# Optimization experiments

Hardware: AMD Instinct MI355X
Metric: run time of the kernel (lower is better)

The kernel has to match this reference:

```python
import jax, jax.numpy as jnp
import numpy as np

B, N, J = 2, 2048, 2048
DIM, HEADS, DH = 1024, 16, 64
INNER = HEADS * DH          # 1024
FF_INNER = 4 * DIM          # 4096
EPS = 1e-5


def layernorm(x, g, b):
    mu = jnp.mean(x, axis=-1, keepdims=True)
    var = jnp.var(x, axis=-1, keepdims=True)
    return (x - mu) * jax.lax.rsqrt(var + EPS) * g + b


def setup_inputs() -> dict:
    key = jax.random.key(0)
    ks = jax.random.split(key, 8)
    s = 0.02
    return {
        "x": jax.random.normal(ks[0], (B, N, DIM), jnp.float32),
        "context": jax.random.normal(ks[1], (B, J, DIM), jnp.float32),
        "norm_g": jnp.ones((DIM,), jnp.float32),
        "norm_b": jnp.zeros((DIM,), jnp.float32),
        "cnorm_g": jnp.ones((DIM,), jnp.float32),
        "cnorm_b": jnp.zeros((DIM,), jnp.float32),
        "Wq": jax.random.normal(ks[2], (DIM, INNER), jnp.float32) * s,
        "Wkv": jax.random.normal(ks[3], (DIM, 2 * DH), jnp.float32) * s,
        "Wo": jax.random.normal(ks[4], (INNER, DIM), jnp.float32) * s,
        "Wff1": jax.random.normal(ks[5], (DIM, 2 * FF_INNER), jnp.float32) * s,
        "Wff2": jax.random.normal(ks[6], (FF_INNER, DIM), jnp.float32) * s,
    }


def reference(x, context, norm_g, norm_b, cnorm_g, cnorm_b, Wq, Wkv, Wo, Wff1, Wff2):
    scale = DH ** -0.5
    xn = layernorm(x, norm_g, norm_b)                      # [b, n, dim]
    cn = layernorm(context, cnorm_g, cnorm_b)              # [b, j, dim]

    q = (xn @ Wq).reshape(B, N, HEADS, DH) * scale         # [b, n, h, dh]
    kv = cn @ Wkv                                          # [b, j, 2*dh]
    k, v = kv[..., :DH], kv[..., DH:]                      # shared across heads (MQA)

    sim = jnp.einsum('bihd,bjd->bhij', q, k)               # [b, h, n, j]
    attn = jax.nn.softmax(sim, axis=-1)                    # amax-stabilized internally
    out = jnp.einsum('bhij,bjd->bihd', attn, v)            # [b, n, h, dh]
    out = out.reshape(B, N, INNER) @ Wo                    # [b, n, dim]

    # parallel SwiGLU FF on the normed input, residual-added
    ff = xn @ Wff1                                         # [b, n, 2*ff_inner]
    a, gate = ff[..., :FF_INNER], ff[..., FF_INNER:]
    out = out + (jax.nn.silu(gate) * a) @ Wff2
    return out
```

## Files before the change

kernel.cpp:

```cpp
#include <hip/hip_runtime.h>
#include <stdint.h>

typedef unsigned short u16;
typedef __attribute__((ext_vector_type(8))) short short8;
typedef __attribute__((ext_vector_type(4))) float f32x4;
typedef __attribute__((ext_vector_type(16))) float f32x16;

#define GPTR(p) ((const __attribute__((address_space(1))) void*)(p))
#define SPTR(p) ((__attribute__((address_space(3))) void*)(p))
#define GLDS16(g, l) __builtin_amdgcn_global_load_lds(GPTR(g), SPTR(l), 16, 0, 0)

static __device__ __forceinline__ float bf2f(u16 u) {
  union { unsigned int i; float f; } c; c.i = ((unsigned int)u) << 16; return c.f;
}
static __device__ __forceinline__ u16 f2bf(float f) {
  union { float f; unsigned int u; } c; c.f = f;
  unsigned int r = 0x7fffu + ((c.u >> 16) & 1u);
  return (u16)((c.u + r) >> 16);
}
static __device__ __forceinline__ unsigned cvtpk(float a, float b) {
  unsigned r;
  asm volatile("v_cvt_pk_bf16_f32 %0, %1, %2" : "=v"(r) : "v"(a), "v"(b));
  return r;
}
static __device__ __forceinline__ int swz4(int row, int c) { return c ^ ((row >> 1) & 3); }

__global__ __launch_bounds__(256) void ln_kernel(
    const float* __restrict__ x, const float* __restrict__ ctx,
    const float* __restrict__ g, const float* __restrict__ b,
    const float* __restrict__ cg, const float* __restrict__ cb,
    u16* __restrict__ xn, u16* __restrict__ cn)
{
  const int row = blockIdx.x;
  const float* src; const float* gg; const float* bb; u16* dst;
  if (row < 4096) { src = x + (size_t)row * 1024; gg = g;  bb = b;  dst = xn + (size_t)row * 1024; }
  else            { src = ctx + (size_t)(row - 4096) * 1024; gg = cg; bb = cb; dst = cn + (size_t)(row - 4096) * 1024; }
  const int t = threadIdx.x;
  float4 v = *(const float4*)&src[t * 4];
  float s  = v.x + v.y + v.z + v.w;
  float s2 = v.x * v.x + v.y * v.y + v.z * v.z + v.w * v.w;
  #pragma unroll
  for (int off = 1; off < 64; off <<= 1) { s += __shfl_xor(s, off); s2 += __shfl_xor(s2, off); }
  __shared__ float ls[4], ls2[4];
  const int w = t >> 6;
  if ((t & 63) == 0) { ls[w] = s; ls2[w] = s2; }
  __syncthreads();
  s  = ls[0] + ls[1] + ls[2] + ls[3];
  s2 = ls2[0] + ls2[1] + ls2[2] + ls2[3];
  const float mu   = s * (1.0f / 1024.0f);
  const float var  = s2 * (1.0f / 1024.0f) - mu * mu;
  const float rstd = rsqrtf(var + 1e-5f);
  float xv[4] = { v.x, v.y, v.z, v.w };
  u16 o[4];
  #pragma unroll
  for (int i = 0; i < 4; ++i)
    o[i] = f2bf((xv[i] - mu) * rstd * gg[t * 4 + i] + bb[t * 4 + i]);
  uint2 pv;
  pv.x = (unsigned)o[0] | ((unsigned)o[1] << 16);
  pv.y = (unsigned)o[2] | ((unsigned)o[3] << 16);
  *(uint2*)&dst[t * 4] = pv;
}

__global__ __launch_bounds__(256) void transpose_k(
    const float* __restrict__ in, u16* __restrict__ out, int R, int C, int ldo, float scale)
{
  __shared__ float tile[64][65];
  const int c0 = blockIdx.x * 64, r0 = blockIdx.y * 64;
  const int t = threadIdx.x;
  const int tr = t >> 4, tc = (t & 15) * 4;
  #pragma unroll
  for (int i = 0; i < 4; ++i) {
    int r = tr + i * 16;
    float4 v = *(const float4*)&in[(size_t)(r0 + r) * C + c0 + tc];
    tile[r][tc + 0] = v.x; tile[r][tc + 1] = v.y; tile[r][tc + 2] = v.z; tile[r][tc + 3] = v.w;
  }
  __syncthreads();
  #pragma unroll
  for (int i = 0; i < 2; ++i) {
    int c  = (t >> 3) + i * 32;
    int rb = (t & 7) * 8;
    union { u16 s[8]; uint4 v; } pk;
    #pragma unroll
    for (int u = 0; u < 8; ++u) pk.s[u] = f2bf(tile[rb + u][c] * scale);
    *(uint4*)&out[(size_t)(c0 + c) * ldo + r0 + rb] = pk.v;
  }
}

__global__ __launch_bounds__(256) void transpose_ff1(
    const float* __restrict__ in, u16* __restrict__ out)
{
  __shared__ float tile[64][65];
  const int c0 = blockIdx.x * 64, r0 = blockIdx.y * 64;
  const int t = threadIdx.x;
  const int tr = t >> 4, tc = (t & 15) * 4;
  #pragma unroll
  for (int i = 0; i < 4; ++i) {
    int r = tr + i * 16;
    float4 v = *(const float4*)&in[(size_t)(r0 + r) * 8192 + c0 + tc];
    tile[r][tc + 0] = v.x; tile[r][tc + 1] = v.y; tile[r][tc + 2] = v.z; tile[r][tc + 3] = v.w;
  }
  __syncthreads();
  #pragma unroll
  for (int i = 0; i < 2; ++i) {
    int c  = (t >> 3) + i * 32;
    int rb = (t & 7) * 8;
    const int gc = c0 + c;
    int j, add16;
    if (gc < 4096) { j = gc; add16 = 0; } else { j = gc - 4096; add16 = 16; }
    const int row = ((j >> 7) << 8) + (((j >> 5) & 3) << 6) + (((j >> 4) & 1) << 5) + add16 + (j & 15);
    union { u16 s[8]; uint4 v; } pk;
    #pragma unroll
    for (int u = 0; u < 8; ++u) pk.s[u] = f2bf(tile[rb + u][c]);
    *(uint4*)&out[(size_t)row * 1024 + r0 + rb] = pk.v;
  }
}

#define MM32(MQ, M, NN) acc[MQ][M][NN] = __builtin_amdgcn_mfma_f32_16x16x32_bf16(af##M, bf##NN, acc[MQ][M][NN], 0, 0, 0)
#define MFMA16_32(MQ) \
  MM32(MQ,0,0); MM32(MQ,0,1); MM32(MQ,0,2); MM32(MQ,0,3); \
  MM32(MQ,1,0); MM32(MQ,1,1); MM32(MQ,1,2); MM32(MQ,1,3); \
  MM32(MQ,2,0); MM32(MQ,2,1); MM32(MQ,2,2); MM32(MQ,2,3); \
  MM32(MQ,3,0); MM32(MQ,3,1); MM32(MQ,3,2); MM32(MQ,3,3)

#define SA32(SBUF, H, KT) GLDS16(gA32[H] + ((size_t)(KT) << 5), SBUF + (size_t)((H) * 64 + w16o) * 32)
#define SB32(SBUF, H, KT) GLDS16(gB32[H] + ((size_t)(KT) << 5), SBUF + (size_t)((H) * 128 + w16o2) * 32)

#define DSB32(PB_) do { \
  bf0 = *(const short8*)(PB_ + 0    + cks); bf1 = *(const short8*)(PB_ + 512  + cks); \
  bf2 = *(const short8*)(PB_ + 1024 + cks); bf3 = *(const short8*)(PB_ + 1536 + cks); \
} while (0)

#define PC32(PA_, MQ, STAGE_STMT, GATE_STMT) do { \
  af0 = *(const short8*)(PA_ + (MQ) * 2048 + 0    + cks); \
  af1 = *(const short8*)(PA_ + (MQ) * 2048 + 512  + cks); \
  af2 = *(const short8*)(PA_ + (MQ) * 2048 + 1024 + cks); \
  af3 = *(const short8*)(PA_ + (MQ) * 2048 + 1536 + cks); \
  STAGE_STMT; \
  __builtin_amdgcn_s_barrier(); \
  asm volatile("s_waitcnt lgkmcnt(0)" ::: "memory"); \
  __builtin_amdgcn_s_setprio(1); \
  MFMA16_32(MQ); \
  __builtin_amdgcn_s_setprio(0); \
  GATE_STMT; \
  __builtin_amdgcn_s_barrier(); \
} while (0)

#define GATE3 asm volatile("s_waitcnt vmcnt(3)" ::: "memory")
#define GATE0 asm volatile("s_waitcnt vmcnt(0)" ::: "memory")

__global__ __launch_bounds__(512, 2) void gemm32_ff(
    const u16* __restrict__ A, const u16* __restrict__ BT, u16* __restrict__ Ho,
    int M, int N, int Ktot)
{
  __shared__ u16 sh[2][2][8192];
  const int nbm = M >> 8;
  const int nwg = gridDim.x;
  const int bid = blockIdx.x;
  const int o = (bid & 7) * (nwg >> 3) + (bid >> 3);
  const int bm = o % nbm, bn = o / nbm;
  const int NI = Ktot >> 6;

  const int t = threadIdx.x, w = t >> 6, lane = t & 63;
  const int wr = w >> 2, wc = w & 3;
  const int lr = lane & 15, lg = lane >> 4;
  const int l4 = lane >> 2, sl = lane & 3;
  const int w16o  = w * 16 + ((w >= 4) ? 64 : 0);
  const int w16o2 = w * 16;

  const u16* gA32[2]; const u16* gB32[2];
  #pragma unroll
  for (int h = 0; h < 2; ++h) {
    const int rowA = h * 64 + w16o + l4;
    gA32[h] = A + (size_t)(bm * 256 + rowA) * Ktot + (size_t)((sl ^ ((rowA >> 1) & 3)) * 8);
    const int rowB = h * 128 + w16o2 + l4;
    gB32[h] = BT + (size_t)(bn * 256 + rowB) * Ktot + (size_t)((sl ^ ((rowB >> 1) & 3)) * 8);
  }
  u16* sA0 = &sh[0][0][0]; u16* sA1 = &sh[1][0][0];
  u16* sB0 = &sh[0][1][0]; u16* sB1 = &sh[1][1][0];
  const int cks = (lg ^ ((lr >> 1) & 3)) * 8;
  const u16* pA_b0 = sA0 + (wr * 128 + lr) * 32;
  const u16* pA_b1 = sA1 + (wr * 128 + lr) * 32;
  const u16* pB_b0 = sB0 + (wc * 64 + lr) * 32;
  const u16* pB_b1 = sB1 + (wc * 64 + lr) * 32;

  f32x4 acc[2][4][4];
  const f32x4 z4 = { 0.f, 0.f, 0.f, 0.f };
  #pragma unroll
  for (int a = 0; a < 2; ++a)
    #pragma unroll
    for (int b = 0; b < 4; ++b)
      #pragma unroll
      for (int c = 0; c < 4; ++c) acc[a][b][c] = z4;
  short8 af0, af1, af2, af3;
  short8 bf0, bf1, bf2, bf3;

  SA32(sA0, 0, 0); SA32(sA0, 1, 0); SB32(sB0, 0, 0); SB32(sB0, 1, 0);
  SB32(sB1, 0, 1); SB32(sB1, 1, 1); SA32(sA1, 0, 1);
  GATE3;
  __builtin_amdgcn_s_barrier();

  for (int i = 0; i < NI; ++i) {
    const bool st = (i < NI - 1);
    const int X = 2 * i + 2, Y = 2 * i + 3;
    DSB32(pB_b0);
    PC32(pA_b0, 0, SA32(sA1, 1, 2 * i + 1), );
    PC32(pA_b0, 1,
         if (st) { SB32(sB0, 0, X); SB32(sB0, 1, X); SA32(sA0, 0, X); },
         if (st) { GATE3; } else { GATE0; });
    DSB32(pB_b1);
    PC32(pA_b1, 0, if (st) { SA32(sA0, 1, X); }, );
    PC32(pA_b1, 1,
         if (st) { SB32(sB1, 0, Y); SB32(sB1, 1, Y); SA32(sA1, 0, Y); },
         if (st) { GATE3; });
  }

  const int colb = 1024 + bn * 128 + wc * 32 + lr;
  #pragma unroll
  for (int mq = 0; mq < 2; ++mq)
    #pragma unroll
    for (int m = 0; m < 4; ++m)
      #pragma unroll
      for (int rr = 0; rr < 4; ++rr) {
        const int row = bm * 256 + wr * 128 + mq * 64 + m * 16 + lg * 4 + rr;
        #pragma unroll
        for (int n2 = 0; n2 < 2; ++n2) {
          const float a = acc[mq][m][2 * n2][rr];
          const float gt = acc[mq][m][2 * n2 + 1][rr];
          const float h = a * gt / (1.0f + __expf(-gt));
          Ho[(size_t)row * 5120 + colb + n2 * 16] = f2bf(h);
        }
      }
}

#define MM1(MQ, M, NN, BF) acc[MQ][M][NN] = __builtin_amdgcn_mfma_f32_16x16x32_bf16(af##M, BF, acc[MQ][M][NN], 0, 0, 0)
#define MFMA16(MQ, KS) \
  MM1(MQ,0,0,bf##KS##0); MM1(MQ,0,1,bf##KS##1); MM1(MQ,0,2,bf##KS##2); MM1(MQ,0,3,bf##KS##3); \
  MM1(MQ,1,0,bf##KS##0); MM1(MQ,1,1,bf##KS##1); MM1(MQ,1,2,bf##KS##2); MM1(MQ,1,3,bf##KS##3); \
  MM1(MQ,2,0,bf##KS##0); MM1(MQ,2,1,bf##KS##1); MM1(MQ,2,2,bf##KS##2); MM1(MQ,2,3,bf##KS##3); \
  MM1(MQ,3,0,bf##KS##0); MM1(MQ,3,1,bf##KS##1); MM1(MQ,3,2,bf##KS##2); MM1(MQ,3,3,bf##KS##3)

#define SG_A(SBUF, H, KT) do { \
    GLDS16(gA[H][0] + ((size_t)(KT) << 6), SBUF + ((H) * 64 + w16o) * 64); \
    GLDS16(gA[H][1] + ((size_t)(KT) << 6), SBUF + ((H) * 64 + w16o + 8) * 64); \
  } while (0)
#define SG_B(SBUF, H, KT) do { \
    GLDS16(gB[H][0] + ((size_t)(KT) << 6), SBUF + ((H) * 128 + w16o2) * 64); \
    GLDS16(gB[H][1] + ((size_t)(KT) << 6), SBUF + ((H) * 128 + w16o2 + 8) * 64); \
  } while (0)

#define DS_B(PB_) do { \
  bf00 = *(const short8*)(PB_ + 0    + cks0); bf01 = *(const short8*)(PB_ + 1024 + cks0); \
  bf02 = *(const short8*)(PB_ + 2048 + cks0); bf03 = *(const short8*)(PB_ + 3072 + cks0); \
  bf10 = *(const short8*)(PB_ + 0    + cks1); bf11 = *(const short8*)(PB_ + 1024 + cks1); \
  bf12 = *(const short8*)(PB_ + 2048 + cks1); bf13 = *(const short8*)(PB_ + 3072 + cks1); \
} while (0)

#define P_CORE(PA_, MQ, KS, STAGE_STMT, PREB_STMT, GATE_STMT) do { \
  af0 = *(const short8*)(PA_ + (MQ) * 4096 + 0    + cks##KS); \
  af1 = *(const short8*)(PA_ + (MQ) * 4096 + 1024 + cks##KS); \
  af2 = *(const short8*)(PA_ + (MQ) * 4096 + 2048 + cks##KS); \
  af3 = *(const short8*)(PA_ + (MQ) * 4096 + 3072 + cks##KS); \
  STAGE_STMT; \
  PREB_STMT; \
  __builtin_amdgcn_s_barrier(); \
  asm volatile("s_waitcnt lgkmcnt(0)" ::: "memory"); \
  __builtin_amdgcn_s_setprio(1); \
  MFMA16(MQ, KS); \
  __builtin_amdgcn_s_setprio(0); \
  GATE_STMT; \
  __builtin_amdgcn_s_barrier(); \
} while (0)

#define GATE6 asm volatile("s_waitcnt vmcnt(6)" ::: "memory")
#define HINT8 asm volatile("s_waitcnt lgkmcnt(8)" ::: "memory")

__global__ __launch_bounds__(512, 2) void gemm64_sk(
    const u16* __restrict__ A, const u16* __restrict__ BT, u16* __restrict__ C,
    int M, int N, int Ktot, int Kslice)
{
  __shared__ u16 sh[2][2][16384];
  const int nbn = N >> 8;
  const int nwg = gridDim.x;
  const int bid = blockIdx.x;
  const int o = (bid & 7) * (nwg >> 3) + (bid >> 3);
  const int bn = o % nbn, bm = o / nbn;
  const int kbase = blockIdx.y * Kslice;
  const int NI = Kslice >> 7;

  const int t = threadIdx.x, w = t >> 6, lane = t & 63;
  const int wr = w >> 2, wc = w & 3;
  const int lr = lane & 15, lg = lane >> 4;
  const int r8 = lane >> 3, ch = lane & 7;
  const int clog = ch ^ r8;
  const int w16o  = w * 16 + ((w >= 4) ? 64 : 0);
  const int w16o2 = w * 16;

  const u16* gA[2][2]; const u16* gB[2][2];
  #pragma unroll
  for (int h = 0; h < 2; ++h)
    #pragma unroll
    for (int qq = 0; qq < 2; ++qq) {
      gA[h][qq] = A  + (size_t)(bm * 256 + h * 64  + w16o  + qq * 8 + r8) * Ktot + kbase + clog * 8;
      gB[h][qq] = BT + (size_t)(bn * 256 + h * 128 + w16o2 + qq * 8 + r8) * Ktot + kbase + clog * 8;
    }
  u16* sA0 = &sh[0][0][0]; u16* sA1 = &sh[1][0][0];
  u16* sB0 = &sh[0][1][0]; u16* sB1 = &sh[1][1][0];
  const int cks0 = ((0 + lg) ^ (lr & 7)) * 8;
  const int cks1 = ((4 + lg) ^ (lr & 7)) * 8;
  const u16* pA_b0 = sA0 + (wr * 128 + lr) * 64;
  const u16* pA_b1 = sA1 + (wr * 128 + lr) * 64;
  const u16* pB_b0 = sB0 + (wc * 64 + lr) * 64;
  const u16* pB_b1 = sB1 + (wc * 64 + lr) * 64;

  f32x4 acc[2][4][4];
  const f32x4 z4 = { 0.f, 0.f, 0.f, 0.f };
  #pragma unroll
  for (int a = 0; a < 2; ++a)
    #pragma unroll
    for (int b = 0; b < 4; ++b)
      #pragma unroll
      for (int c = 0; c < 4; ++c) acc[a][b][c] = z4;
  short8 af0, af1, af2, af3;
  short8 bf00, bf01, bf02, bf03, bf10, bf11, bf12, bf13;

  SG_B(sB0, 0, 0); SG_B(sB0, 1, 0); SG_A(sA0, 0, 0); SG_A(sA0, 1, 0);
  SG_B(sB1, 0, 1); SG_B(sB1, 1, 1); SG_A(sA1, 0, 1);
  GATE6;
  __builtin_amdgcn_s_barrier();

  for (int i = 0; i < NI; ++i) {
    const int k2 = 2 * i;
    const bool st = (i < NI - 1);
    DS_B(pB_b0);
    P_CORE(pA_b0, 0, 0, SG_A(sA1, 1, k2 + 1), HINT8, );
    P_CORE(pA_b0, 1, 0, if (st) SG_B(sB0, 0, k2 + 2), , );
    P_CORE(pA_b0, 0, 1, if (st) SG_B(sB0, 1, k2 + 2), , );
    P_CORE(pA_b0, 1, 1, if (st) SG_A(sA0, 0, k2 + 2), ,
           if (st) { GATE6; } else { GATE0; });
    DS_B(pB_b1);
    P_CORE(pA_b1, 0, 0, if (st) SG_A(sA0, 1, k2 + 2), HINT8, );
    P_CORE(pA_b1, 1, 0, if (st) SG_B(sB1, 0, k2 + 3), , );
    P_CORE(pA_b1, 0, 1, if (st) SG_B(sB1, 1, k2 + 3), , );
    P_CORE(pA_b1, 1, 1, if (st) SG_A(sA1, 0, k2 + 3), ,
           if (st) { GATE6; });
  }

  u16* Co = C + (size_t)blockIdx.y * M * N;
  #pragma unroll
  for (int mq = 0; mq < 2; ++mq)
    #pragma unroll
    for (int m = 0; m < 4; ++m)
      #pragma unroll
      for (int n = 0; n < 4; ++n)
        #pragma unroll
        for (int rr = 0; rr < 4; ++rr) {
          const int row = bm * 256 + wr * 128 + mq * 64 + m * 16 + lg * 4 + rr;
          const int col = bn * 256 + wc * 64 + n * 16 + lr;
          Co[(size_t)row * N + col] = f2bf(acc[mq][m][n][rr]);
        }
}

__global__ __launch_bounds__(256) void gemm_bt_sk(
    const u16* __restrict__ A, const u16* __restrict__ BT, u16* __restrict__ Cp,
    int M, int N, int Kslice, int Ktot)
{
  __shared__ u16 As[128 * 32];
  __shared__ u16 Bs[128 * 32];
  const int bm = blockIdx.y, bn = blockIdx.x, z = blockIdx.z;
  const int t = threadIdx.x;
  const int w = t >> 6, lane = t & 63;
  const int wr = w >> 1, wc = w & 1;
  const int lr = lane & 15, lkc = lane >> 4;

  f32x4 acc[4][4];
  const f32x4 z4 = { 0.f, 0.f, 0.f, 0.f };
  #pragma unroll
  for (int mi = 0; mi < 4; ++mi)
    #pragma unroll
    for (int ni = 0; ni < 4; ++ni) acc[mi][ni] = z4;

  const int kbase = z * Kslice;
  const int i0 = t, i1 = t + 256;
  const int r0 = i0 >> 2, k0 = swz4(r0, i0 & 3) * 8;
  const int r1 = i1 >> 2, k1 = swz4(r1, i1 & 3) * 8;
  const u16* a0 = A + (size_t)(bm * 128 + r0) * Ktot + kbase + k0;
  const u16* a1 = A + (size_t)(bm * 128 + r1) * Ktot + kbase + k1;
  const u16* b0 = BT + (size_t)(bn * 128 + r0) * Ktot + kbase + k0;
  const u16* b1 = BT + (size_t)(bn * 128 + r1) * Ktot + kbase + k1;
  u16* As0 = As + (size_t)w * 512;
  u16* As1 = As + (size_t)(w + 4) * 512;
  u16* Bs0 = Bs + (size_t)w * 512;
  u16* Bs1 = Bs + (size_t)(w + 4) * 512;

  const int nk = Kslice >> 5;
  for (int kt = 0; kt < nk; ++kt) {
    __syncthreads();
    GLDS16(a0, As0); GLDS16(a1, As1); GLDS16(b0, Bs0); GLDS16(b1, Bs1);
    a0 += 32; a1 += 32; b0 += 32; b1 += 32;
    __syncthreads();
    short8 af[4], bf[4];
    #pragma unroll
    for (int mi = 0; mi < 4; ++mi) {
      int row = wr * 64 + mi * 16 + lr;
      af[mi] = *(const short8*)&As[row * 32 + swz4(row, lkc) * 8];
    }
    #pragma unroll
    for (int ni = 0; ni < 4; ++ni) {
      int row = wc * 64 + ni * 16 + lr;
      bf[ni] = *(const short8*)&Bs[row * 32 + swz4(row, lkc) * 8];
    }
    #pragma unroll
    for (int mi = 0; mi < 4; ++mi)
      #pragma unroll
      for (int ni = 0; ni < 4; ++ni)
        acc[mi][ni] = __builtin_amdgcn_mfma_f32_16x16x32_bf16(af[mi], bf[ni], acc[mi][ni], 0, 0, 0);
  }

  u16* Cz = Cp + (size_t)z * M * N;
  const int row0 = bm * 128 + wr * 64, col0 = bn * 128 + wc * 64;
  const int rsub = (lane >> 4) * 4;
  #pragma unroll
  for (int mi = 0; mi < 4; ++mi)
    #pragma unroll
    for (int ni = 0; ni < 4; ++ni)
      #pragma unroll
      for (int r = 0; r < 4; ++r)
        Cz[(size_t)(row0 + mi * 16 + rsub + r) * N + (col0 + ni * 16 + lr)] = f2bf(acc[mi][ni][r]);
}

__global__ __launch_bounds__(256) void reduce_kv(const u16* __restrict__ part, u16* __restrict__ out)
{
  const size_t base = ((size_t)blockIdx.x * 256 + threadIdx.x) * 8;
  float s[8] = { 0.f, 0.f, 0.f, 0.f, 0.f, 0.f, 0.f, 0.f };
  #pragma unroll
  for (int zz = 0; zz < 8; ++zz) {
    const short8 v = *(const short8*)&part[(size_t)zz * 524288 + base];
    #pragma unroll
    for (int i = 0; i < 8; ++i) s[i] += bf2f((u16)v[i]);
  }
  union { u16 o[8]; uint4 v; } pk;
  #pragma unroll
  for (int i = 0; i < 8; ++i) pk.o[i] = f2bf(s[i]);
  *(uint4*)&out[base] = pk.v;
}

__global__ __launch_bounds__(256) void reduce_out(const u16* __restrict__ part, float* __restrict__ out)
{
  const size_t base = ((size_t)blockIdx.x * 256 + threadIdx.x) * 8;
  float s[8] = { 0.f, 0.f, 0.f, 0.f, 0.f, 0.f, 0.f, 0.f };
  #pragma unroll
  for (int zz = 0; zz < 4; ++zz) {
    const short8 v = *(const short8*)&part[(size_t)zz * 4194304 + base];
    #pragma unroll
    for (int i = 0; i < 8; ++i) s[i] += bf2f((u16)v[i]);
  }
  f32x4 lo = { s[0], s[1], s[2], s[3] };
  f32x4 hi = { s[4], s[5], s[6], s[7] };
  *(f32x4*)&out[base] = lo;
  *(f32x4*)&out[base + 4] = hi;
}

__global__ __launch_bounds__(256) void attn_kernel(
    const u16* __restrict__ q, const u16* __restrict__ kv, u16* __restrict__ o)
{
  __shared__ u16 Ks[128 * 64];
  __shared__ u16 Vt[64 * 128];
  __shared__ u16 Ps[4][32 * 128];
  const int b = blockIdx.z, hb = blockIdx.y, qb = blockIdx.x;
  const int t = threadIdx.x, w = t >> 6, lane = t & 63;
  const int q32 = lane & 31, hl = lane >> 5;
  const int hd = hb * 4 + w;

  const size_t qbase = (size_t)b * 2048 + qb * 64;
  short8 qa[2][4];
  #pragma unroll
  for (int t32 = 0; t32 < 2; ++t32)
    #pragma unroll
    for (int dq = 0; dq < 4; ++dq)
      qa[t32][dq] = *(const short8*)&q[(qbase + t32 * 32 + q32) * 1024 + hd * 64 + dq * 16 + hl * 8];

  f32x16 oacc[2][2];
  #pragma unroll
  for (int i = 0; i < 2; ++i)
    #pragma unroll
    for (int j = 0; j < 2; ++j)
      #pragma unroll
      for (int r = 0; r < 16; ++r) oacc[i][j][r] = 0.f;
  float m_[2] = { -1e30f, -1e30f }, l_[2] = { 0.f, 0.f };

  const size_t kvb = (size_t)b * 2048 * 128;
  const int vd0 = (t & 7) * 8;
  const int vodd = (t >> 3) & 1;
  u16* Pw = &Ps[w][0];

  uint4 vhold[4];
  #pragma unroll
  for (int c = 0; c < 4; ++c) {
    const int vj = (c * 256 + t) >> 3;
    vhold[c] = *(const uint4*)&kv[kvb + (size_t)vj * 128 + 64 + vd0];
  }

  for (int jt = 0; jt < 16; ++jt) {
    __syncthreads();
    #pragma unroll
    for (int n = 0; n < 4; ++n) {
      const int cc = n * 256 + w * 64;
      const int ccl = cc + lane;
      const int row = ccl >> 3, lc = (ccl & 7) ^ (row & 7);
      GLDS16(&kv[kvb + (size_t)(jt * 128 + row) * 128 + lc * 8], Ks + (size_t)cc * 8);
    }
    #pragma unroll
    for (int c = 0; c < 4; ++c) {
      const int seg = c * 256 + t;
      const int vj = seg >> 3;
      const int jp = vj >> 1;
      const uint4 vv = vhold[c];
      uint4 pvv;
      pvv.x = __shfl_xor((int)vv.x, 8);
      pvv.y = __shfl_xor((int)vv.y, 8);
      pvv.z = __shfl_xor((int)vv.z, 8);
      pvv.w = __shfl_xor((int)vv.w, 8);
      const unsigned ow[4] = { vv.x, vv.y, vv.z, vv.w };
      const unsigned pw[4] = { pvv.x, pvv.y, pvv.z, pvv.w };
      if (!vodd) {
        #pragma unroll
        for (int u = 0; u < 4; ++u) {
          const int d = vd0 + u;
          const unsigned own = (u & 1) ? (ow[u >> 1] >> 16) : (ow[u >> 1] & 0xffffu);
          const unsigned par = (u & 1) ? (pw[u >> 1] >> 16) : (pw[u >> 1] & 0xffffu);
          const int byteoff = d * 256 + ((4 * jp) ^ (((d & 7) ^ ((d >> 3) & 7)) << 4));
          *(unsigned*)((char*)Vt + byteoff) = own | (par << 16);
        }
      } else {
        #pragma unroll
        for (int u = 0; u < 4; ++u) {
          const int ue = u + 4;
          const int d = vd0 + ue;
          const unsigned own = (ue & 1) ? (ow[ue >> 1] >> 16) : (ow[ue >> 1] & 0xffffu);
          const unsigned par = (ue & 1) ? (pw[ue >> 1] >> 16) : (pw[ue >> 1] & 0xffffu);
          const int byteoff = d * 256 + ((4 * jp) ^ (((d & 7) ^ ((d >> 3) & 7)) << 4));
          *(unsigned*)((char*)Vt + byteoff) = par | (own << 16);
        }
      }
    }
    __builtin_amdgcn_sched_barrier(0);
    if (jt < 15) {
      #pragma unroll
      for (int c = 0; c < 4; ++c) {
        const int vj = (c * 256 + t) >> 3;
        vhold[c] = *(const uint4*)&kv[kvb + (size_t)((jt + 1) * 128 + vj) * 128 + 64 + vd0];
      }
      asm volatile("s_waitcnt vmcnt(4) lgkmcnt(0)" ::: "memory");
    } else {
      asm volatile("s_waitcnt vmcnt(0) lgkmcnt(0)" ::: "memory");
    }
    __builtin_amdgcn_s_barrier();
    __builtin_amdgcn_sched_barrier(0);

    #pragma unroll
    for (int t32 = 0; t32 < 2; ++t32) {
      f32x16 s[4];
      #pragma unroll
      for (int j32 = 0; j32 < 4; ++j32)
        #pragma unroll
        for (int r = 0; r < 16; ++r) s[j32][r] = 0.f;
      __builtin_amdgcn_s_setprio(1);
      #pragma unroll
      for (int j32 = 0; j32 < 4; ++j32) {
        const int row = j32 * 32 + q32;
        #pragma unroll
        for (int dq = 0; dq < 4; ++dq) {
          const int slot = (dq * 2 + hl) ^ (row & 7);
          const short8 kf = *(const short8*)&Ks[row * 64 + slot * 8];
          s[j32] = __builtin_amdgcn_mfma_f32_32x32x16_bf16(kf, qa[t32][dq], s[j32], 0, 0, 0);
        }
      }
      __builtin_amdgcn_s_setprio(0);
      float mt = -1e30f;
      #pragma unroll
      for (int j32 = 0; j32 < 4; ++j32)
        #pragma unroll
        for (int r = 0; r < 16; ++r) mt = fmaxf(mt, s[j32][r]);
      mt = fmaxf(mt, __shfl_xor(mt, 32));
      const bool noresc = (bool)__all(mt <= m_[t32] + 8.0f);
      float nm = m_[t32];
      if (!noresc) {
        nm = fmaxf(m_[t32], mt);
        const float alpha = __expf(m_[t32] - nm);
        m_[t32] = nm;
        l_[t32] *= alpha;
        #pragma unroll
        for (int d32 = 0; d32 < 2; ++d32)
          #pragma unroll
          for (int r = 0; r < 16; ++r) oacc[t32][d32][r] *= alpha;
      }
      float lsum = 0.f;
      #pragma unroll
      for (int j32 = 0; j32 < 4; ++j32) {
        float p[16];
        #pragma unroll
        for (int r = 0; r < 16; ++r) { p[r] = __expf(s[j32][r] - nm); lsum += p[r]; }
        #pragma unroll
        for (int g = 0; g < 4; ++g) {
          const unsigned lo = cvtpk(p[4 * g + 0], p[4 * g + 1]);
          const unsigned hi = cvtpk(p[4 * g + 2], p[4 * g + 3]);
          const int j2 = j32 * 64 + 16 * g + 8 * hl;
          const int byteoff = q32 * 256 + (j2 ^ ((q32 & 7) << 4));
          uint2 wv; wv.x = lo; wv.y = hi;
          *(uint2*)((char*)Pw + byteoff) = wv;
        }
      }
      lsum += __shfl_xor(lsum, 32);
      l_[t32] += lsum;
      short8 pf[8];
      #pragma unroll
      for (int kk = 0; kk < 8; ++kk) {
        const int byteoff = q32 * 256 + ((kk * 32 + hl * 16) ^ ((q32 & 7) << 4));
        pf[kk] = *(const short8*)((const char*)Pw + byteoff);
      }
      __builtin_amdgcn_s_setprio(1);
      #pragma unroll
      for (int d32 = 0; d32 < 2; ++d32) {
        const int dr = d32 * 32 + q32;
        const int vswz = ((dr & 7) ^ ((dr >> 3) & 7)) << 4;
        #pragma unroll
        for (int kk = 0; kk < 8; ++kk) {
          const int byteoff = dr * 256 + ((kk * 32 + hl * 16) ^ vswz);
          const short8 vf = *(const short8*)((const char*)Vt + byteoff);
          oacc[t32][d32] = __builtin_amdgcn_mfma_f32_32x32x16_bf16(vf, pf[kk], oacc[t32][d32], 0, 0, 0);
        }
      }
      __builtin_amdgcn_s_setprio(0);
    }
  }

  float* Ot = (float*)Pw;
  #pragma unroll
  for (int t32 = 0; t32 < 2; ++t32) {
    const float inv = 1.0f / l_[t32];
    #pragma unroll
    for (int d32 = 0; d32 < 2; ++d32) {
      #pragma unroll
      for (int r = 0; r < 16; ++r) {
        const int d = (r & 3) + 8 * (r >> 2) + 4 * hl;
        const int byteoff = q32 * 128 + ((4 * d) ^ ((q32 & 7) << 4));
        *(float*)((char*)Ot + byteoff) = oacc[t32][d32][r] * inv;
      }
      const int qr = lane >> 1, dc = (lane & 1) * 16;
      union { u16 s[16]; uint4 v[2]; } ob;
      #pragma unroll
      for (int cch = 0; cch < 4; ++cch) {
        const int byteoff = qr * 128 + ((4 * (dc + 4 * cch)) ^ ((qr & 7) << 4));
        const f32x4 vv = *(const f32x4*)((const char*)Ot + byteoff);
        ob.s[cch * 4 + 0] = f2bf(vv[0]);
        ob.s[cch * 4 + 1] = f2bf(vv[1]);
        ob.s[cch * 4 + 2] = f2bf(vv[2]);
        ob.s[cch * 4 + 3] = f2bf(vv[3]);
      }
      u16* orow = &o[(qbase + t32 * 32 + qr) * 5120 + hd * 64 + d32 * 32 + dc];
      *(uint4*)orow = ob.v[0];
      *(uint4*)(orow + 8) = ob.v[1];
    }
  }
}

extern "C" void kernel_launch(void* const* d_in, const int* in_sizes, int n_in,
                              void* d_out, int out_size, void* d_ws, size_t ws_size,
                              hipStream_t stream)
{
  const float* x    = (const float*)d_in[0];
  const float* ctx  = (const float*)d_in[1];
  const float* ng   = (const float*)d_in[2];
  const float* nb   = (const float*)d_in[3];
  const float* cg   = (const float*)d_in[4];
  const float* cb   = (const float*)d_in[5];
  const float* Wq   = (const float*)d_in[6];
  const float* Wkv  = (const float*)d_in[7];
  const float* Wo   = (const float*)d_in[8];
  const float* Wff1 = (const float*)d_in[9];
  const float* Wff2 = (const float*)d_in[10];

  u16* p = (u16*)d_ws;
  u16* WqT   = p; p += (size_t)1024 * 1024;
  u16* W2T   = p; p += (size_t)8192 * 1024;
  u16* WkvT  = p; p += (size_t)128 * 1024;
  u16* WcT   = p; p += (size_t)1024 * 5120;
  u16* kvbuf = p; p += (size_t)4096 * 128;
  u16* aoh   = p; p += (size_t)4096 * 5120;
  u16* xn    = p; p += (size_t)4096 * 1024;
  u16* cn    = p; p += (size_t)4096 * 1024;
  u16* qbuf  = p; p += (size_t)4096 * 1024;
  u16* kvpart = W2T;
  u16* ffpart = xn;
  (void)in_sizes; (void)n_in; (void)out_size; (void)ws_size;

  ln_kernel<<<8192, 256, 0, stream>>>(x, ctx, ng, nb, cg, cb, xn, cn);

  transpose_k<<<dim3(16, 16),  256, 0, stream>>>(Wq,   WqT,        1024, 1024, 1024, 0.125f);
  transpose_ff1<<<dim3(128, 16), 256, 0, stream>>>(Wff1, W2T);
  transpose_k<<<dim3(2, 16),   256, 0, stream>>>(Wkv,  WkvT,       1024, 128,  1024, 1.0f);
  transpose_k<<<dim3(16, 16),  256, 0, stream>>>(Wo,   WcT,        1024, 1024, 5120, 1.0f);
  transpose_k<<<dim3(16, 64),  256, 0, stream>>>(Wff2, WcT + 1024, 4096, 1024, 5120, 1.0f);

  gemm32_ff<<<dim3(512), 512, 0, stream>>>(xn, W2T, aoh, 4096, 8192, 1024);
  gemm_bt_sk<<<dim3(8, 32, 1), 256, 0, stream>>>(xn, WqT, qbuf, 4096, 1024, 1024, 1024);
  gemm_bt_sk<<<dim3(1, 32, 8), 256, 0, stream>>>(cn, WkvT, kvpart, 4096, 128, 128, 1024);
  reduce_kv<<<256, 256, 0, stream>>>(kvpart, kvbuf);
  attn_kernel<<<dim3(32, 4, 2), 256, 0, stream>>>(qbuf, kvbuf, aoh);
  gemm64_sk<<<dim3(64, 4), 512, 0, stream>>>(aoh, WcT, ffpart, 4096, 1024, 5120, 1280);
  reduce_out<<<2048, 256, 0, stream>>>(ffpart, (float*)d_out);
}
```

Measured before the change: 285.4 us.

## Split attention query halves across separate waves with 512-thread blocks

```diff
diff --git a/kernel.cpp b/kernel.cpp
--- a/kernel.cpp
+++ b/kernel.cpp
@@ -460,58 +460,55 @@
   *(f32x4*)&out[base + 4] = hi;
 }
 
-__global__ __launch_bounds__(256) void attn_kernel(
+__global__ __launch_bounds__(512, 1) void attn_kernel(
     const u16* __restrict__ q, const u16* __restrict__ kv, u16* __restrict__ o)
 {
   __shared__ u16 Ks[128 * 64];
   __shared__ u16 Vt[64 * 128];
-  __shared__ u16 Ps[4][32 * 128];
+  __shared__ u16 Ps[8][32 * 128];
   const int b = blockIdx.z, hb = blockIdx.y, qb = blockIdx.x;
   const int t = threadIdx.x, w = t >> 6, lane = t & 63;
   const int q32 = lane & 31, hl = lane >> 5;
-  const int hd = hb * 4 + w;
+  const int hd = hb * 4 + (w >> 1);
+  const int t32 = w & 1;
 
   const size_t qbase = (size_t)b * 2048 + qb * 64;
-  short8 qa[2][4];
-  #pragma unroll
-  for (int t32 = 0; t32 < 2; ++t32)
-    #pragma unroll
-    for (int dq = 0; dq < 4; ++dq)
-      qa[t32][dq] = *(const short8*)&q[(qbase + t32 * 32 + q32) * 1024 + hd * 64 + dq * 16 + hl * 8];
-
-  f32x16 oacc[2][2];
-  #pragma unroll
-  for (int i = 0; i < 2; ++i)
-    #pragma unroll
-    for (int j = 0; j < 2; ++j)
-      #pragma unroll
-      for (int r = 0; r < 16; ++r) oacc[i][j][r] = 0.f;
-  float m_[2] = { -1e30f, -1e30f }, l_[2] = { 0.f, 0.f };
+  short8 qa[4];
+  #pragma unroll
+  for (int dq = 0; dq < 4; ++dq)
+    qa[dq] = *(const short8*)&q[(qbase + t32 * 32 + q32) * 1024 + hd * 64 + dq * 16 + hl * 8];
+
+  f32x16 oacc[2];
+  #pragma unroll
+  for (int j = 0; j < 2; ++j)
+    #pragma unroll
+    for (int r = 0; r < 16; ++r) oacc[j][r] = 0.f;
+  float m_ = -1e30f, l_ = 0.f;
 
   const size_t kvb = (size_t)b * 2048 * 128;
   const int vd0 = (t & 7) * 8;
   const int vodd = (t >> 3) & 1;
   u16* Pw = &Ps[w][0];
 
-  uint4 vhold[4];
-  #pragma unroll
-  for (int c = 0; c < 4; ++c) {
-    const int vj = (c * 256 + t) >> 3;
+  uint4 vhold[2];
+  #pragma unroll
+  for (int c = 0; c < 2; ++c) {
+    const int vj = (c * 512 + t) >> 3;
     vhold[c] = *(const uint4*)&kv[kvb + (size_t)vj * 128 + 64 + vd0];
   }
 
   for (int jt = 0; jt < 16; ++jt) {
     __syncthreads();
     #pragma unroll
-    for (int n = 0; n < 4; ++n) {
-      const int cc = n * 256 + w * 64;
+    for (int n = 0; n < 2; ++n) {
+      const int cc = n * 512 + w * 64;
       const int ccl = cc + lane;
       const int row = ccl >> 3, lc = (ccl & 7) ^ (row & 7);
       GLDS16(&kv[kvb + (size_t)(jt * 128 + row) * 128 + lc * 8], Ks + (size_t)cc * 8);
     }
     #pragma unroll
-    for (int c = 0; c < 4; ++c) {
-      const int seg = c * 256 + t;
+    for (int c = 0; c < 2; ++c) {
+      const int seg = c * 512 + t;
       const int vj = seg >> 3;
       const int jp = vj >> 1;
       const uint4 vv = vhold[c];
@@ -546,121 +543,115 @@
     __builtin_amdgcn_sched_barrier(0);
     if (jt < 15) {
       #pragma unroll
-      for (int c = 0; c < 4; ++c) {
-        const int vj = (c * 256 + t) >> 3;
+      for (int c = 0; c < 2; ++c) {
+        const int vj = (c * 512 + t) >> 3;
         vhold[c] = *(const uint4*)&kv[kvb + (size_t)((jt + 1) * 128 + vj) * 128 + 64 + vd0];
       }
-      asm volatile("s_waitcnt vmcnt(4) lgkmcnt(0)" ::: "memory");
+      asm volatile("s_waitcnt vmcnt(2) lgkmcnt(0)" ::: "memory");
     } else {
       asm volatile("s_waitcnt vmcnt(0) lgkmcnt(0)" ::: "memory");
     }
     __builtin_amdgcn_s_barrier();
     __builtin_amdgcn_sched_barrier(0);
 
-    #pragma unroll
-    for (int t32 = 0; t32 < 2; ++t32) {
-      f32x16 s[4];
-      #pragma unroll
-      for (int j32 = 0; j32 < 4; ++j32)
+    f32x16 s[4];
+    #pragma unroll
+    for (int j32 = 0; j32 < 4; ++j32)
+      #pragma unroll
+      for (int r = 0; r < 16; ++r) s[j32][r] = 0.f;
+    __builtin_amdgcn_s_setprio(1);
+    #pragma unroll
+    for (int j32 = 0; j32 < 4; ++j32) {
+      const int row = j32 * 32 + q32;
+      #pragma unroll
+      for (int dq = 0; dq < 4; ++dq) {
+        const int slot = (dq * 2 + hl) ^ (row & 7);
+        const short8 kf = *(const short8*)&Ks[row * 64 + slot * 8];
+        s[j32] = __builtin_amdgcn_mfma_f32_32x32x16_bf16(kf, qa[dq], s[j32], 0, 0, 0);
+      }
+    }
+    __builtin_amdgcn_s_setprio(0);
+    float mt = -1e30f;
+    #pragma unroll
+    for (int j32 = 0; j32 < 4; ++j32)
+      #pragma unroll
+      for (int r = 0; r < 16; ++r) mt = fmaxf(mt, s[j32][r]);
+    mt = fmaxf(mt, __shfl_xor(mt, 32));
+    const bool noresc = (bool)__all(mt <= m_ + 8.0f);
+    float nm = m_;
+    if (!noresc) {
+      nm = fmaxf(m_, mt);
+      const float alpha = __expf(m_ - nm);
+      m_ = nm;
+      l_ *= alpha;
+      #pragma unroll
+      for (int d32 = 0; d32 < 2; ++d32)
         #pragma unroll
-        for (int r = 0; r < 16; ++r) s[j32][r] = 0.f;
-      __builtin_amdgcn_s_setprio(1);
-      #pragma unroll
-      for (int j32 = 0; j32 < 4; ++j32) {
-        const int row = j32 * 32 + q32;
-        #pragma unroll
-        for (int dq = 0; dq < 4; ++dq) {
-          const int slot = (dq * 2 + hl) ^ (row & 7);
-          const short8 kf = *(const short8*)&Ks[row * 64 + slot * 8];
-          s[j32] = __builtin_amdgcn_mfma_f32_32x32x16_bf16(kf, qa[t32][dq], s[j32], 0, 0, 0);
-        }
+        for (int r = 0; r < 16; ++r) oacc[d32][r] *= alpha;
+    }
+    float lsum = 0.f;
+    #pragma unroll
+    for (int j32 = 0; j32 < 4; ++j32) {
+      float p[16];
+      #pragma unroll
+      for (int r = 0; r < 16; ++r) { p[r] = __expf(s[j32][r] - nm); lsum += p[r]; }
+      #pragma unroll
+      for (int g = 0; g < 4; ++g) {
+        const unsigned lo = cvtpk(p[4 * g + 0], p[4 * g + 1]);
+        const unsigned hi = cvtpk(p[4 * g + 2], p[4 * g + 3]);
+        const int j2 = j32 * 64 + 16 * g + 8 * hl;
+        const int byteoff = q32 * 256 + (j2 ^ ((q32 & 7) << 4));
+        uint2 wv; wv.x = lo; wv.y = hi;
+        *(uint2*)((char*)Pw + byteoff) = wv;
       }
-      __builtin_amdgcn_s_setprio(0);
-      float mt = -1e30f;
-      #pragma unroll
-      for (int j32 = 0; j32 < 4; ++j32)
-        #pragma unroll
-        for (int r = 0; r < 16; ++r) mt = fmaxf(mt, s[j32][r]);
-      mt = fmaxf(mt, __shfl_xor(mt, 32));
-      const bool noresc = (bool)__all(mt <= m_[t32] + 8.0f);
-      float nm = m_[t32];
-      if (!noresc) {
-        nm = fmaxf(m_[t32], mt);
-        const float alpha = __expf(m_[t32] - nm);
-        m_[t32] = nm;
-        l_[t32] *= alpha;
-        #pragma unroll
-        for (int d32 = 0; d32 < 2; ++d32)
-          #pragma unroll
-          for (int r = 0; r < 16; ++r) oacc[t32][d32][r] *= alpha;
+    }
+    lsum += __shfl_xor(lsum, 32);
+    l_ += lsum;
+    short8 pf[8];
+    #pragma unroll
+    for (int kk = 0; kk < 8; ++kk) {
+      const int byteoff = q32 * 256 + ((kk * 32 + hl * 16) ^ ((q32 & 7) << 4));
+      pf[kk] = *(const short8*)((const char*)Pw + byteoff);
+    }
+    __builtin_amdgcn_s_setprio(1);
+    #pragma unroll
+    for (int d32 = 0; d32 < 2; ++d32) {
+      const int dr = d32 * 32 + q32;
+      const int vswz = ((dr & 7) ^ ((dr >> 3) & 7)) << 4;
+      #pragma unroll
+      for (int kk = 0; kk < 8; ++kk) {
+        const int byteoff = dr * 256 + ((kk * 32 + hl * 16) ^ vswz);
+        const short8 vf = *(const short8*)((const char*)Vt + byteoff);
+        oacc[d32] = __builtin_amdgcn_mfma_f32_32x32x16_bf16(vf, pf[kk], oacc[d32], 0, 0, 0);
       }
-      float lsum = 0.f;
-      #pragma unroll
-      for (int j32 = 0; j32 < 4; ++j32) {
-        float p[16];
-        #pragma unroll
-        for (int r = 0; r < 16; ++r) { p[r] = __expf(s[j32][r] - nm); lsum += p[r]; }
-        #pragma unroll
-        for (int g = 0; g < 4; ++g) {
-          const unsigned lo = cvtpk(p[4 * g + 0], p[4 * g + 1]);
-          const unsigned hi = cvtpk(p[4 * g + 2], p[4 * g + 3]);
-          const int j2 = j32 * 64 + 16 * g + 8 * hl;
-          const int byteoff = q32 * 256 + (j2 ^ ((q32 & 7) << 4));
-          uint2 wv; wv.x = lo; wv.y = hi;
-          *(uint2*)((char*)Pw + byteoff) = wv;
-        }
-      }
-      lsum += __shfl_xor(lsum, 32);
-      l_[t32] += lsum;
-      short8 pf[8];
-      #pragma unroll
-      for (int kk = 0; kk < 8; ++kk) {
-        const int byteoff = q32 * 256 + ((kk * 32 + hl * 16) ^ ((q32 & 7) << 4));
-        pf[kk] = *(const short8*)((const char*)Pw + byteoff);
-      }
-      __builtin_amdgcn_s_setprio(1);
-      #pragma unroll
-      for (int d32 = 0; d32 < 2; ++d32) {
-        const int dr = d32 * 32 + q32;
-        const int vswz = ((dr & 7) ^ ((dr >> 3) & 7)) << 4;
-        #pragma unroll
-        for (int kk = 0; kk < 8; ++kk) {
-          const int byteoff = dr * 256 + ((kk * 32 + hl * 16) ^ vswz);
-          const short8 vf = *(const short8*)((const char*)Vt + byteoff);
-          oacc[t32][d32] = __builtin_amdgcn_mfma_f32_32x32x16_bf16(vf, pf[kk], oacc[t32][d32], 0, 0, 0);
-        }
-      }
-      __builtin_amdgcn_s_setprio(0);
-    }
+    }
+    __builtin_amdgcn_s_setprio(0);
   }
 
   float* Ot = (float*)Pw;
-  #pragma unroll
-  for (int t32 = 0; t32 < 2; ++t32) {
-    const float inv = 1.0f / l_[t32];
-    #pragma unroll
-    for (int d32 = 0; d32 < 2; ++d32) {
-      #pragma unroll
-      for (int r = 0; r < 16; ++r) {
-        const int d = (r & 3) + 8 * (r >> 2) + 4 * hl;
-        const int byteoff = q32 * 128 + ((4 * d) ^ ((q32 & 7) << 4));
-        *(float*)((char*)Ot + byteoff) = oacc[t32][d32][r] * inv;
-      }
-      const int qr = lane >> 1, dc = (lane & 1) * 16;
-      union { u16 s[16]; uint4 v[2]; } ob;
-      #pragma unroll
-      for (int cch = 0; cch < 4; ++cch) {
-        const int byteoff = qr * 128 + ((4 * (dc + 4 * cch)) ^ ((qr & 7) << 4));
-        const f32x4 vv = *(const f32x4*)((const char*)Ot + byteoff);
-        ob.s[cch * 4 + 0] = f2bf(vv[0]);
-        ob.s[cch * 4 + 1] = f2bf(vv[1]);
-        ob.s[cch * 4 + 2] = f2bf(vv[2]);
-        ob.s[cch * 4 + 3] = f2bf(vv[3]);
-      }
-      u16* orow = &o[(qbase + t32 * 32 + qr) * 5120 + hd * 64 + d32 * 32 + dc];
-      *(uint4*)orow = ob.v[0];
-      *(uint4*)(orow + 8) = ob.v[1];
-    }
+  const float inv = 1.0f / l_;
+  #pragma unroll
+  for (int d32 = 0; d32 < 2; ++d32) {
+    #pragma unroll
+    for (int r = 0; r < 16; ++r) {
+      const int d = (r & 3) + 8 * (r >> 2) + 4 * hl;
+      const int byteoff = q32 * 128 + ((4 * d) ^ ((q32 & 7) << 4));
+      *(float*)((char*)Ot + byteoff) = oacc[d32][r] * inv;
+    }
+    const int qr = lane >> 1, dc = (lane & 1) * 16;
+    union { u16 s[16]; uint4 v[2]; } ob;
+    #pragma unroll
+    for (int cch = 0; cch < 4; ++cch) {
+      const int byteoff = qr * 128 + ((4 * (dc + 4 * cch)) ^ ((qr & 7) << 4));
+      const f32x4 vv = *(const f32x4*)((const char*)Ot + byteoff);
+      ob.s[cch * 4 + 0] = f2bf(vv[0]);
+      ob.s[cch * 4 + 1] = f2bf(vv[1]);
+      ob.s[cch * 4 + 2] = f2bf(vv[2]);
+      ob.s[cch * 4 + 3] = f2bf(vv[3]);
+    }
+    u16* orow = &o[(qbase + t32 * 32 + qr) * 5120 + hd * 64 + d32 * 32 + dc];
+    *(uint4*)orow = ob.v[0];
+    *(uint4*)(orow + 8) = ob.v[1];
   }
 }
 
@@ -706,7 +697,7 @@
   gemm_bt_sk<<<dim3(8, 32, 1), 256, 0, stream>>>(xn, WqT, qbuf, 4096, 1024, 1024, 1024);
   gemm_bt_sk<<<dim3(1, 32, 8), 256, 0, stream>>>(cn, WkvT, kvpart, 4096, 128, 128, 1024);
   reduce_kv<<<256, 256, 0, stream>>>(kvpart, kvbuf);
-  attn_kernel<<<dim3(32, 4, 2), 256, 0, stream>>>(qbuf, kvbuf, aoh);
+  attn_kernel<<<dim3(32, 4, 2), 512, 0, stream>>>(qbuf, kvbuf, aoh);
   gemm64_sk<<<dim3(64, 4), 512, 0, stream>>>(aoh, WcT, ffpart, 4096, 1024, 5120, 1280);
   reduce_out<<<2048, 256, 0, stream>>>(ffpart, (float*)d_out);
 }
```

Result: faster. 263.5 us (-7.7%).
